# Performance work log

Hardware: AMD Instinct MI355X
Metric: run time of the kernel (lower is better)

## Reference

```python
import jax, jax.numpy as jnp
import numpy as np
import math

N_HEAD = 8


def _rope(x):
    # x: [B, H, S, D]; lucidrains rotary_embedding_torch default: interleaved pairs, theta=10000
    D = x.shape[-1]
    S = x.shape[-2]
    inv_freq = 1.0 / (10000.0 ** (jnp.arange(0, D, 2, dtype=jnp.float32) / D))  # [D/2]
    t = jnp.arange(S, dtype=jnp.float32)
    freqs = jnp.repeat(t[:, None] * inv_freq[None, :], 2, axis=-1)  # [S, D] interleaved repeat
    cos = jnp.cos(freqs).astype(x.dtype)
    sin = jnp.sin(freqs).astype(x.dtype)
    xp = x.reshape(*x.shape[:-1], D // 2, 2)
    rot = jnp.stack((-xp[..., 1], xp[..., 0]), axis=-1).reshape(x.shape)  # rotate_half (interleaved)
    return x * cos + rot * sin


def _row_linear(x, Wo):
    # faithful RowLinear: transpose then flat-reshape back (a real permutation), linear, inverse shuffle
    B, S, P = x.shape
    E = Wo.shape[0]
    x = jnp.swapaxes(x, 1, 2).reshape(B, S, P)
    x = jnp.einsum('bsp,ep->bse', x, Wo)  # [B, S, E]
    x = x.reshape(B, E, -1)  # [B, E, S]
    return jnp.swapaxes(x, 1, 2)  # [B, S, E]


def setup_inputs() -> dict:
    key = jax.random.key(0)
    k0, k1, k2, k3, k4 = jax.random.split(key, 5)
    B, S, E, P = 4, 2048, 1024, 1024
    std = 1.0 / math.sqrt(E)
    return {
        'emb': jax.random.normal(k0, (B, S, E), dtype=jnp.float32),
        'W1': jax.random.normal(k1, (P, E), dtype=jnp.float32) * std,
        'W2': jax.random.normal(k2, (P, E), dtype=jnp.float32) * std,
        'W3': jax.random.normal(k3, (P, E), dtype=jnp.float32) * std,
        'Wo': jax.random.normal(k4, (E, P), dtype=jnp.float32) * std,
    }


def reference(emb, W1, W2, W3, Wo):
    B, S, E = emb.shape
    P = W1.shape[0]
    H = N_HEAD
    D = P // H
    q = jnp.einsum('bse,pe->bsp', emb, W1).reshape(B, H, S, D)  # raw view split (as in source)
    k = jnp.einsum('bse,pe->bsp', emb, W2).reshape(B, H, S, D)
    v = jnp.einsum('bse,pe->bsp', emb, W3).reshape(B, H, S, D)
    q = _rope(q)
    k = _rope(k)
    scores = jnp.einsum('bhqd,bhkd->bhqk', q, k).astype(jnp.float32) / math.sqrt(H)
    attn = jax.nn.softmax(scores, axis=-1).astype(v.dtype)
    out = jnp.einsum('bhqk,bhkd->bhqd', attn, v)  # [B, H, S, D]
    out = jnp.swapaxes(out, 1, 2).reshape(B, S, P)
    return _row_linear(out, Wo)
```

## Files before the change

### kernel.cpp

```cpp
#include <hip/hip_runtime.h>

typedef float f32x4 __attribute__((ext_vector_type(4)));
typedef float f32x16 __attribute__((ext_vector_type(16)));
typedef __bf16 bf16x8 __attribute__((ext_vector_type(8)));

__device__ __forceinline__ unsigned short f2bf(float f) {
  unsigned int u = __float_as_uint(f);
  u = (u + 0x7FFFu + ((u >> 16) & 1u)) >> 16;
  return (unsigned short)u;
}
__device__ __forceinline__ float bf2f(unsigned short u) {
  return __uint_as_float((unsigned int)u << 16);
}

__device__ __forceinline__ f32x4 mfma16(bf16x8 a, bf16x8 b, f32x4 c) {
  return __builtin_amdgcn_mfma_f32_16x16x32_bf16(a, b, c, 0, 0, 0);
}
__device__ __forceinline__ f32x16 mfma32(bf16x8 a, bf16x8 b, f32x16 c) {
  return __builtin_amdgcn_mfma_f32_32x32x16_bf16(a, b, c, 0, 0, 0);
}

__device__ __forceinline__ unsigned int cvtpk_bf16(float a, float b) {
  unsigned int r;
  asm("v_cvt_pk_bf16_f32 %0, %1, %2" : "=v"(r) : "v"(a), "v"(b));
  return r;
}
__device__ __forceinline__ void pl32swap(unsigned int& a, unsigned int& b) {
  asm("v_permlane32_swap_b32 %0, %1" : "+v"(a), "+v"(b));
}

__device__ __forceinline__ void load8_bf16(const unsigned short* p, unsigned short* d) {
  *(uint4*)d = *(const uint4*)p;
}
__device__ __forceinline__ void load8_bf16(const float* p, unsigned short* d) {
  float4 a = *(const float4*)p;
  float4 b = *(const float4*)(p + 4);
  __align__(16) unsigned short t[8] = {f2bf(a.x), f2bf(a.y), f2bf(a.z), f2bf(a.w),
                                       f2bf(b.x), f2bf(b.y), f2bf(b.z), f2bf(b.w)};
  *(uint4*)d = *(uint4*)t;
}

__device__ __forceinline__ void gload_lds16(const unsigned short* g, unsigned short* l) {
  __builtin_amdgcn_global_load_lds(
      (const __attribute__((address_space(1))) void*)g,
      (__attribute__((address_space(3))) void*)l, 16, 0, 0);
}

__device__ __forceinline__ void drain_barrier() {
  asm volatile("s_waitcnt vmcnt(0)" ::: "memory");
  __builtin_amdgcn_sched_barrier(0);
  __builtin_amdgcn_s_barrier();
  __builtin_amdgcn_sched_barrier(0);
}

__device__ __forceinline__ void wait2_barrier() {
  asm volatile("s_waitcnt vmcnt(2)" ::: "memory");
  __builtin_amdgcn_sched_barrier(0);
  __builtin_amdgcn_s_barrier();
  __builtin_amdgcn_sched_barrier(0);
}

__global__ __launch_bounds__(256) void convert_gen(const float* __restrict__ src,
                                                   unsigned short* __restrict__ dst) {
  int idx = (blockIdx.x * 256 + threadIdx.x) * 8;
  __align__(16) unsigned short t[8];
  load8_bf16(src + idx, t);
  *(uint4*)(dst + idx) = *(uint4*)t;
}

__global__ __launch_bounds__(256) void convert_w3(const float* __restrict__ W1,
                                                  const float* __restrict__ W2,
                                                  const float* __restrict__ W3,
                                                  unsigned short* __restrict__ dst) {
  int i = blockIdx.x;
  int sel = i >> 9;
  const float* src = (sel == 0) ? W1 : (sel == 1) ? W2 : W3;
  int w = i & 511;
  int t = threadIdx.x;
  int p = 2 * w + (t >> 7);
  int kc = t & 127;
  __align__(16) unsigned short tmp[8];
  load8_bf16(src + (size_t)p * 1024 + kc * 8, tmp);
  int lane = (kc & 3) * 16 + (p & 15);
  size_t idx16 = ((((size_t)(p >> 7) * 32 + (kc >> 2)) * 2 + ((p >> 6) & 1)) * 4 +
                  ((p >> 4) & 3)) * 64 + lane;
  *(uint4*)(dst + (size_t)sel * 1048576 + idx16 * 8) = *(uint4*)tmp;
}

__global__ __launch_bounds__(256) void convert_wo(const float* __restrict__ Wo,
                                                  unsigned short* __restrict__ dst) {
  int w = blockIdx.x;
  int t = threadIdx.x;
  int p = 2 * w + (t >> 7);
  int kc = t & 127;
  __align__(16) unsigned short tmp[8];
  load8_bf16(Wo + (size_t)p * 1024 + kc * 8, tmp);
  int lane = (kc & 3) * 16 + (p & 15);
  size_t idx16 = ((((size_t)(p >> 7) * 32 + (kc >> 2)) * 2 + ((p >> 6) & 1)) * 4 +
                  ((p >> 4) & 3)) * 64 + lane;
  *(uint4*)(dst + idx16 * 8) = *(uint4*)tmp;
}

__global__ __launch_bounds__(256) void gemm_qkv(const unsigned short* __restrict__ A,
                                                const unsigned short* __restrict__ WBf,
                                                unsigned short* __restrict__ q,
                                                unsigned short* __restrict__ k,
                                                unsigned short* __restrict__ v) {
  __shared__ __align__(16) unsigned short As[3][128][32];
  const int t = threadIdx.x;
  const int lane = t & 63;
  const int wid = t >> 6;
  const int quad = lane >> 4;
  const int l16 = lane & 15;
  const int wm = (wid >> 1) << 6;
  const int wn = (wid & 1) << 6;
  const int sel = blockIdx.x >> 3;
  const int nb = blockIdx.x & 7;
  const int mbase = blockIdx.y * 128;
  unsigned short* C = (sel == 0) ? q : (sel == 1) ? k : v;

  const unsigned short* aSrc0 = A + (size_t)(mbase + (t >> 2)) * 1024 + ((t & 3) << 3);
  const unsigned short* aSrc1 = A + (size_t)(mbase + 64 + (t >> 2)) * 1024 + ((t & 3) << 3);
  unsigned short* aDst0 = &As[0][0][0] + t * 8;
  unsigned short* aDst1 = &As[0][0][0] + 2048 + t * 8;
  auto stageA = [&](int k0, int p) {
    gload_lds16(aSrc0 + k0, aDst0 + p * 4096);
    gload_lds16(aSrc1 + k0, aDst1 + p * 4096);
  };

  const unsigned short* pB = WBf + (size_t)sel * 1048576 +
                             ((size_t)(nb * 64 + (wid & 1)) * 4) * 512 + lane * 8;

  f32x4 acc[4][4] = {};

  stageA(0, 0);
  stageA(32, 1);
  asm volatile("s_waitcnt vmcnt(2)" ::: "memory");
  __builtin_amdgcn_sched_barrier(0);
  __builtin_amdgcn_s_barrier();
  __builtin_amdgcn_sched_barrier(0);

  int p = 0;
  for (int k0 = 0; k0 < 1024; k0 += 32) {
    bf16x8 bfr[4];
#pragma unroll
    for (int nt = 0; nt < 4; ++nt) bfr[nt] = *(const bf16x8*)(pB + nt * 512);
    pB += 4096;
    if (k0 + 64 < 1024) stageA(k0 + 64, p == 0 ? 2 : p - 1);
    bf16x8 af[4];
#pragma unroll
    for (int mt = 0; mt < 4; ++mt)
      af[mt] = *(const bf16x8*)(&As[p][wm + mt * 16 + l16][quad * 8]);
#pragma unroll
    for (int nt = 0; nt < 4; ++nt)
#pragma unroll
      for (int mt = 0; mt < 4; ++mt)
        acc[mt][nt] = mfma16(af[mt], bfr[nt], acc[mt][nt]);
    wait2_barrier();
    p = (p == 2) ? 0 : p + 1;
  }

  const bool rope = (sel < 2);
#pragma unroll
  for (int mt = 0; mt < 4; ++mt) {
#pragma unroll
    for (int nt = 0; nt < 4; ++nt) {
#pragma unroll
      for (int r = 0; r < 4; ++r) {
        int row_g = mbase + wm + mt * 16 + quad * 4 + r;
        int col_g = (nb << 7) + wn + nt * 16 + l16;
        float val = acc[mt][nt][r];
        if (rope) {
          float other = __shfl_xor(val, 1);
          int s = (((row_g & 2047) << 3) + (col_g >> 7)) & 2047;
          int d = col_g & 127;
          float invf = __expf(-0.14391156f * (float)(d >> 1));
          float ang = (float)s * invf;
          float sv, cv;
          __sincosf(ang, &sv, &cv);
          val = (d & 1) ? (val * cv + other * sv) : (val * cv - other * sv);
        }
        C[(size_t)row_g * 1024 + col_g] = f2bf(val);
      }
    }
  }
}

__global__ __launch_bounds__(256) void transpose_v(const unsigned short* __restrict__ Vn,
                                                   unsigned short* __restrict__ VT) {
  __shared__ __align__(16) unsigned short tile[64][72];
  const int t = threadIdx.x;
  const int s0 = blockIdx.x * 64;
  const int d0 = blockIdx.y * 64;
  const int bh = blockIdx.z;
  const size_t base = (size_t)bh * (2048 * 128);
#pragma unroll
  for (int i = 0; i < 2; ++i) {
    int c = t + (i << 8);
    int sr = c >> 3;
    int dc = (c & 7) << 3;
    *(uint4*)(&tile[sr][dc]) = *(const uint4*)(Vn + base + (size_t)(s0 + sr) * 128 + d0 + dc);
  }
  __syncthreads();
#pragma unroll
  for (int i = 0; i < 2; ++i) {
    int c = t + (i << 8);
    int dr = c >> 3;
    int sc = (c & 7) << 3;
    __align__(16) unsigned short tmp[8];
#pragma unroll
    for (int j = 0; j < 8; ++j) tmp[j] = tile[sc + j][dr];
    *(uint4*)(VT + base + (size_t)(d0 + dr) * 2048 + s0 + sc) = *(uint4*)tmp;
  }
}

__global__ __launch_bounds__(256) void gemm_out(const unsigned short* __restrict__ OT,
                                                const unsigned short* __restrict__ Bf,
                                                float* __restrict__ C) {
  __shared__ __align__(16) char smem_raw[34816];
  const int t = threadIdx.x;
  const int lane = t & 63;
  const int wid = t >> 6;
  const int quad = lane >> 4;
  const int l16 = lane & 15;
  const int wm = (wid >> 1) << 6;
  const int wn = (wid & 1) << 6;
  const int mbase = blockIdx.y * 128;
  const int nbx = blockIdx.x;

  const unsigned short* aSrcs[2];
#pragma unroll
  for (int i = 0; i < 2; ++i) {
    int c = t + (i << 8);
    int row = c >> 2;
    int col = (c & 3) << 3;
    int R = mbase + row;
    int b = R >> 11;
    int ii = R & 2047;
    aSrcs[i] = OT + (size_t)(b * 8 + (ii >> 8)) * (128 * 2048) +
               (size_t)((ii >> 1) & 127) * 2048 + ((ii & 1) << 10) + col;
  }
  unsigned short* smE = (unsigned short*)smem_raw;
  auto stageA = [&](int k0, int p) {
    gload_lds16(aSrcs[0] + k0, smE + p * 4096 + t * 8);
    gload_lds16(aSrcs[1] + k0, smE + p * 4096 + 2048 + t * 8);
  };

  const unsigned short* pB = Bf + ((size_t)(nbx * 64 + (wid & 1)) * 4) * 512 + lane * 8;

  f32x4 acc[4][4] = {};

  stageA(0, 0);
  stageA(32, 1);
  asm volatile("s_waitcnt vmcnt(2)" ::: "memory");
  __builtin_amdgcn_sched_barrier(0);
  __builtin_amdgcn_s_barrier();
  __builtin_amdgcn_sched_barrier(0);

  int p = 0;
  for (int k0 = 0; k0 < 1024; k0 += 32) {
    bf16x8 bfr[4];
#pragma unroll
    for (int nt = 0; nt < 4; ++nt) bfr[nt] = *(const bf16x8*)(pB + nt * 512);
    pB += 4096;
    if (k0 + 64 < 1024) stageA(k0 + 64, p == 0 ? 2 : p - 1);
    auto As = (unsigned short(*)[32])(smem_raw + p * 8192);
    bf16x8 af[4];
#pragma unroll
    for (int mt = 0; mt < 4; ++mt)
      af[mt] = *(const bf16x8*)(&As[wm + mt * 16 + l16][quad * 8]);
#pragma unroll
    for (int nt = 0; nt < 4; ++nt)
#pragma unroll
      for (int mt = 0; mt < 4; ++mt)
        acc[mt][nt] = mfma16(af[mt], bfr[nt], acc[mt][nt]);
    wait2_barrier();
    p = (p == 2) ? 0 : p + 1;
  }

  float(*Ts)[68] = (float(*)[68])smem_raw;
  const int b = mbase >> 11;
  const int ebase = (mbase & 2047) >> 1;
#pragma unroll
  for (int p2 = 0; p2 < 2; ++p2) {
    __syncthreads();
#pragma unroll
    for (int mt = 0; mt < 4; ++mt)
#pragma unroll
      for (int nt = 0; nt < 4; ++nt)
#pragma unroll
        for (int rr = p2; rr < 4; rr += 2) {
          int col_local = wn + nt * 16 + l16;
          int row_local = wm + mt * 16 + quad * 4 + rr;
          Ts[col_local][row_local >> 1] = acc[mt][nt][rr];
        }
    __syncthreads();
    int srow = t >> 1;
    int e0 = (t & 1) << 5;
    float* dst = C + (size_t)b * 2097152 +
                 (size_t)(p2 * 1024 + nbx * 128 + srow) * 1024 + ebase + e0;
#pragma unroll
    for (int j = 0; j < 8; ++j)
      ((float4*)dst)[j] = *(const float4*)&Ts[srow][e0 + j * 4];
  }
}

__global__ __launch_bounds__(256, 2) void flash_attn(const unsigned short* __restrict__ Q,
                                                     const unsigned short* __restrict__ Kg,
                                                     const unsigned short* __restrict__ VTg,
                                                     unsigned short* __restrict__ OT) {
  __shared__ __align__(16) char sm[65536];
  const int t = threadIdx.x;
  const int lane = t & 63;
  const int wid = t >> 6;
  const int l31 = lane & 31;
  const int hi = lane >> 5;
  const int x16 = (l31 & 7) << 4;
  const int i = blockIdx.x;
  const int bh = (i & 7) + ((i >> 3) & 3) * 8;
  const int qbase = (i >> 5) << 7;
  const size_t base = (size_t)bh * (2048 * 128);
  const float scale = 0.3535533905932738f;

  const unsigned short* Kg_b = Kg + base;
  const unsigned short* Vg_b = VTg + base;

  auto issueKV = [&](int kvoff, int pbit) {
    unsigned short* Kl = (unsigned short*)(sm + (pbit << 14));
    unsigned short* Vl = (unsigned short*)(sm + 32768 + (pbit << 14));
#pragma unroll
    for (int j = 0; j < 4; ++j) {
      int c = t + (j << 8);
      int row = c >> 4, ch = c & 15;
      gload_lds16(Kg_b + (size_t)(kvoff + row) * 128 + ((ch ^ (row & 7)) << 3),
                  Kl + c * 8);
      int d = c >> 3, cv = c & 7;
      gload_lds16(Vg_b + (size_t)d * 2048 + kvoff + ((cv ^ (d & 7)) << 3), Vl + c * 8);
    }
  };

  bf16x8 qf[8];
  {
    const unsigned short* qp = Q + base + (size_t)(qbase + wid * 32 + l31) * 128 + hi * 8;
#pragma unroll
    for (int ks = 0; ks < 8; ++ks) qf[ks] = *(const bf16x8*)(qp + ks * 16);
  }

  f32x16 accO[4] = {};
  float m = -__builtin_inff();
  float l = 0.f;

  issueKV(0, 0);
  drain_barrier();

  for (int kv = 0; kv < 2048; kv += 64) {
    const int p = (kv >> 6) & 1;
    if (kv + 64 < 2048) issueKV(kv + 64, p ^ 1);
    const char* Kb = sm + (p << 14);
    const char* Vb = sm + 32768 + (p << 14);

    f32x16 s0 = {}, s1 = {};
#pragma unroll
    for (int ks = 0; ks < 8; ++ks) {
      int cb = (ks * 32 + hi * 16) ^ x16;
      bf16x8 k0 = *(const bf16x8*)(Kb + l31 * 256 + cb);
      bf16x8 k1 = *(const bf16x8*)(Kb + 8192 + l31 * 256 + cb);
      s0 = mfma32(k0, qf[ks], s0);
      s1 = mfma32(k1, qf[ks], s1);
    }

    float t8[8];
#pragma unroll
    for (int r = 0; r < 8; ++r)
      t8[r] = fmaxf(fmaxf(s0[r], s0[r + 8]), fmaxf(s1[r], s1[r + 8]));
#pragma unroll
    for (int d = 4; d > 0; d >>= 1)
#pragma unroll
      for (int r = 0; r < d; ++r) t8[r] = fmaxf(t8[r], t8[r + d]);
    float mx = fmaxf(t8[0], __shfl_xor(t8[0], 32));
    if (__any(mx > m + 16.f)) {
      float mnew = fmaxf(m, mx);
      float alpha = __expf((m - mnew) * scale);
      l *= alpha;
#pragma unroll
      for (int dt = 0; dt < 4; ++dt)
#pragma unroll
        for (int r = 0; r < 16; ++r) accO[dt][r] *= alpha;
      m = mnew;
    }
    float negms = -m * scale;
#pragma unroll
    for (int r = 0; r < 16; ++r) s0[r] = __expf(fmaf(s0[r], scale, negms));
#pragma unroll
    for (int r = 0; r < 16; ++r) s1[r] = __expf(fmaf(s1[r], scale, negms));
#pragma unroll
    for (int r = 0; r < 8; ++r)
      t8[r] = (s0[r] + s0[r + 8]) + (s1[r] + s1[r + 8]);
#pragma unroll
    for (int d = 4; d > 0; d >>= 1)
#pragma unroll
      for (int r = 0; r < d; ++r) t8[r] += t8[r + d];
    l += t8[0] + __shfl_xor(t8[0], 32);

    bf16x8 pfrag[4];
#pragma unroll
    for (int kb = 0; kb < 4; ++kb) {
      const f32x16& S = (kb < 2) ? s0 : s1;
      const int b = (kb & 1) * 8;
      unsigned int a0 = cvtpk_bf16(S[b + 0], S[b + 1]);
      unsigned int a1 = cvtpk_bf16(S[b + 2], S[b + 3]);
      unsigned int a2 = cvtpk_bf16(S[b + 4], S[b + 5]);
      unsigned int a3 = cvtpk_bf16(S[b + 6], S[b + 7]);
      pl32swap(a0, a2);
      pl32swap(a1, a3);
      union { unsigned int u[4]; bf16x8 v; } pu;
      pu.u[0] = a0; pu.u[1] = a1; pu.u[2] = a2; pu.u[3] = a3;
      pfrag[kb] = pu.v;
    }

#pragma unroll
    for (int dt = 0; dt < 4; ++dt) {
#pragma unroll
      for (int kb = 0; kb < 4; ++kb) {
        bf16x8 vfr = *(const bf16x8*)(Vb + l31 * 128 + dt * 4096 +
                                      ((kb * 32 + hi * 16) ^ x16));
        accO[dt] = mfma32(vfr, pfrag[kb], accO[dt]);
      }
    }

    drain_barrier();
  }

  auto To = (unsigned short(*)[136])sm;
  const float invl = 1.f / l;
  const int qloc = wid * 32 + l31;
#pragma unroll
  for (int dt = 0; dt < 4; ++dt)
#pragma unroll
    for (int r = 0; r < 16; ++r) {
      int d = dt * 32 + (r & 3) + ((r >> 2) << 3) + hi * 4;
      To[d][qloc] = f2bf(accO[dt][r] * invl);
    }
  __syncthreads();
  int dr = t >> 1;
  int off = (t & 1) << 6;
  unsigned short* dst = OT + base + (size_t)dr * 2048 + qbase + off;
#pragma unroll
  for (int j = 0; j < 8; ++j)
    ((uint4*)dst)[j] = *(const uint4*)&To[dr][off + j * 8];
}

extern "C" void kernel_launch(void* const* d_in, const int* in_sizes, int n_in,
                              void* d_out, int out_size, void* d_ws, size_t ws_size,
                              hipStream_t stream) {
  const float* emb = (const float*)d_in[0];
  const float* W1  = (const float*)d_in[1];
  const float* W2  = (const float*)d_in[2];
  const float* W3  = (const float*)d_in[3];
  const float* Wo  = (const float*)d_in[4];
  float* out = (float*)d_out;

  const size_t NELEM = (size_t)8 * 1024 * 1024;
  unsigned short* q     = (unsigned short*)d_ws;
  unsigned short* k     = q + NELEM;
  unsigned short* vn    = k + NELEM;
  unsigned short* X     = vn + NELEM;
  unsigned short* oT    = vn;
  unsigned short* vT    = X;
  unsigned short* W123B = X;
  unsigned short* WoB   = X;
  unsigned short* embB  = (unsigned short*)d_out;

  dim3 blk(256, 1, 1);
  convert_w3<<<dim3(1536), blk, 0, stream>>>(W1, W2, W3, W123B);
  convert_gen<<<dim3(4096), blk, 0, stream>>>(emb, embB);
  gemm_qkv<<<dim3(24, 64), blk, 0, stream>>>(embB, W123B, q, k, vn);
  transpose_v<<<dim3(32, 2, 32), blk, 0, stream>>>(vn, vT);
  flash_attn<<<dim3(512, 1, 1), blk, 0, stream>>>(q, k, vT, oT);
  convert_wo<<<dim3(512), blk, 0, stream>>>(Wo, WoB);
  gemm_out<<<dim3(8, 64), blk, 0, stream>>>(oT, WoB, out);
}
```

Baseline: 317.0 us.

## Software-pipeline QK^T one tile ahead of softmax/PV with triple-buffered V

Restructures the flash-attention main loop so that the QK^T MFMAs for the next KV tile are issued before the softmax and PV work of the current tile. This lets matrix and vector/exp work interleave. V gets a third LDS buffer, so a tile's V stays live while the next tiles load, which raises LDS use from 64KB to 80KB per block. The exp is also switched to exp2f with log2e folded into the scale. The larger LDS footprint may lower occupancy below the two blocks per CU requested by launch bounds, and the extra live score registers raise register pressure.

```diff
diff --git a/kernel.cpp b/kernel.cpp
--- a/kernel.cpp
+++ b/kernel.cpp
@@ -309,7 +309,7 @@
                                                      const unsigned short* __restrict__ Kg,
                                                      const unsigned short* __restrict__ VTg,
                                                      unsigned short* __restrict__ OT) {
-  __shared__ __align__(16) char sm[65536];
+  __shared__ __align__(16) char sm[81920];
   const int t = threadIdx.x;
   const int lane = t & 63;
   const int wid = t >> 6;
@@ -320,14 +320,15 @@
   const int bh = (i & 7) + ((i >> 3) & 3) * 8;
   const int qbase = (i >> 5) << 7;
   const size_t base = (size_t)bh * (2048 * 128);
-  const float scale = 0.3535533905932738f;
+  const float sl2 = 0.51006976f;
 
   const unsigned short* Kg_b = Kg + base;
   const unsigned short* Vg_b = VTg + base;
 
-  auto issueKV = [&](int kvoff, int pbit) {
-    unsigned short* Kl = (unsigned short*)(sm + (pbit << 14));
-    unsigned short* Vl = (unsigned short*)(sm + 32768 + (pbit << 14));
+  auto issueKV = [&](int tt) {
+    const int kvoff = tt * 64;
+    unsigned short* Kl = (unsigned short*)(sm + ((tt & 1) << 14));
+    unsigned short* Vl = (unsigned short*)(sm + 32768 + ((tt % 3) << 14));
 #pragma unroll
     for (int j = 0; j < 4; ++j) {
       int c = t + (j << 8);
@@ -350,25 +351,23 @@
   float m = -__builtin_inff();
   float l = 0.f;
 
-  issueKV(0, 0);
-  drain_barrier();
-
-  for (int kv = 0; kv < 2048; kv += 64) {
-    const int p = (kv >> 6) & 1;
-    if (kv + 64 < 2048) issueKV(kv + 64, p ^ 1);
-    const char* Kb = sm + (p << 14);
-    const char* Vb = sm + 32768 + (p << 14);
-
-    f32x16 s0 = {}, s1 = {};
+  auto qk = [&](int kb, f32x16& o0, f32x16& o1) {
+    const char* Kb = sm + (kb << 14);
+    f32x16 a0 = {}, a1 = {};
 #pragma unroll
     for (int ks = 0; ks < 8; ++ks) {
       int cb = (ks * 32 + hi * 16) ^ x16;
       bf16x8 k0 = *(const bf16x8*)(Kb + l31 * 256 + cb);
       bf16x8 k1 = *(const bf16x8*)(Kb + 8192 + l31 * 256 + cb);
-      s0 = mfma32(k0, qf[ks], s0);
-      s1 = mfma32(k1, qf[ks], s1);
-    }
-
+      a0 = mfma32(k0, qf[ks], a0);
+      a1 = mfma32(k1, qf[ks], a1);
+    }
+    o0 = a0;
+    o1 = a1;
+  };
+
+  auto fin_pv = [&](f32x16& s0, f32x16& s1, int vb) {
+    const char* Vb = sm + 32768 + (vb << 14);
     float t8[8];
 #pragma unroll
     for (int r = 0; r < 8; ++r)
@@ -380,7 +379,7 @@
     float mx = fmaxf(t8[0], __shfl_xor(t8[0], 32));
     if (__any(mx > m + 16.f)) {
       float mnew = fmaxf(m, mx);
-      float alpha = __expf((m - mnew) * scale);
+      float alpha = exp2f((m - mnew) * sl2);
       l *= alpha;
 #pragma unroll
       for (int dt = 0; dt < 4; ++dt)
@@ -388,14 +387,13 @@
         for (int r = 0; r < 16; ++r) accO[dt][r] *= alpha;
       m = mnew;
     }
-    float negms = -m * scale;
-#pragma unroll
-    for (int r = 0; r < 16; ++r) s0[r] = __expf(fmaf(s0[r], scale, negms));
-#pragma unroll
-    for (int r = 0; r < 16; ++r) s1[r] = __expf(fmaf(s1[r], scale, negms));
-#pragma unroll
-    for (int r = 0; r < 8; ++r)
-      t8[r] = (s0[r] + s0[r + 8]) + (s1[r] + s1[r + 8]);
+    float negms = -m * sl2;
+#pragma unroll
+    for (int r = 0; r < 16; ++r) s0[r] = exp2f(fmaf(s0[r], sl2, negms));
+#pragma unroll
+    for (int r = 0; r < 16; ++r) s1[r] = exp2f(fmaf(s1[r], sl2, negms));
+#pragma unroll
+    for (int r = 0; r < 8; ++r) t8[r] = (s0[r] + s0[r + 8]) + (s1[r] + s1[r + 8]);
 #pragma unroll
     for (int d = 4; d > 0; d >>= 1)
 #pragma unroll
@@ -427,10 +425,28 @@
         accO[dt] = mfma32(vfr, pfrag[kb], accO[dt]);
       }
     }
-
+  };
+
+  issueKV(0);
+  drain_barrier();
+  issueKV(1);
+  f32x16 sA0, sA1, sB0, sB1;
+  qk(0, sA0, sA1);
+
+  for (int tt = 0; tt < 32; tt += 2) {
     drain_barrier();
-  }
-
+    if (tt + 2 < 32) issueKV(tt + 2);
+    qk((tt + 1) & 1, sB0, sB1);
+    fin_pv(sA0, sA1, tt % 3);
+    if (tt + 2 < 32) {
+      drain_barrier();
+      if (tt + 3 < 32) issueKV(tt + 3);
+      qk(tt & 1, sA0, sA1);
+    }
+    fin_pv(sB0, sB1, (tt + 1) % 3);
+  }
+
+  __syncthreads();
   auto To = (unsigned short(*)[136])sm;
   const float invl = 1.f / l;
   const int qloc = wid * 32 + l31;
```

New measurement: 321.4 us. No clear change (+1.4%).
